# Kernel optimization log

Measured on AMD Instinct MI355X. Metric: run time of the kernel, lower is better.

Reference implementation:

```python
import jax, jax.numpy as jnp
import numpy as np

B, N, C, IC = 8, 4096, 1024, 256
EPS = 1e-5


def setup_inputs() -> dict:
    key = jax.random.key(0)
    ks = jax.random.split(key, 10)
    s = 0.02  # keep activations well-scaled
    return {
        "v": jax.random.normal(ks[0], (B, N, C), jnp.float32),
        "g_w": jax.random.normal(ks[1], (IC, C), jnp.float32) * s,
        "g_b": jax.random.normal(ks[2], (IC,), jnp.float32) * s,
        "theta_w": jax.random.normal(ks[3], (IC, C), jnp.float32) * s,
        "theta_b": jax.random.normal(ks[4], (IC,), jnp.float32) * s,
        "phi_w": jax.random.normal(ks[5], (IC, C), jnp.float32) * s,
        "phi_b": jax.random.normal(ks[6], (IC,), jnp.float32) * s,
        "W_w": jax.random.normal(ks[7], (C, IC), jnp.float32) * s,
        "W_b": jax.random.normal(ks[8], (C,), jnp.float32) * s,
        "bn_gamma": jnp.ones((C,), jnp.float32),
        "bn_beta": jnp.zeros((C,), jnp.float32),
    }


def reference(v, g_w, g_b, theta_w, theta_b, phi_w, phi_b, W_w, W_b, bn_gamma, bn_beta):
    # v: (B, N, C). All Conv1d(k=1) == per-token matmul.
    g_v = jnp.einsum("bnc,ic->bni", v, g_w) + g_b          # (B, N, IC)
    theta_v = jnp.einsum("bnc,ic->bni", v, theta_w) + theta_b
    phi_v = jnp.einsum("bnc,ic->bni", v, phi_w) + phi_b
    n = v.shape[1]
    # Affinity: R = theta @ phi^T, normalized by N (no softmax)
    R = jnp.einsum("bni,bmi->bnm", theta_v, phi_v) / n      # (B, N, N)
    y = jnp.einsum("bnm,bmi->bni", R, g_v)                  # (B, N, IC)
    W_y = jnp.einsum("bni,ci->bnc", y, W_w) + W_b           # (B, N, C)
    # BatchNorm1d training mode: per-channel stats over (B, N), biased var
    mean = jnp.mean(W_y, axis=(0, 1))
    var = jnp.var(W_y, axis=(0, 1))
    W_y = (W_y - mean) * jax.lax.rsqrt(var + EPS) * bn_gamma + bn_beta
    return W_y + v                                          # residual, (B, N, C)
```

## Files before the change

### kernel.cpp

```cpp
#include <hip/hip_runtime.h>
#include <hip/hip_bf16.h>
#include <stdint.h>


using bf16 = __hip_bfloat16;
typedef __attribute__((ext_vector_type(8))) short short8;
typedef __attribute__((ext_vector_type(4))) float f32x4;
typedef __attribute__((ext_vector_type(4))) short short4v;

#define DEVI static __device__ __forceinline__

DEVI float bf2f(unsigned short u) {
  union { unsigned int i; float f; } x; x.i = ((unsigned int)u) << 16; return x.f;
}
DEVI unsigned short f2bf(float f) {
  __hip_bfloat16 h = __float2bfloat16(f);
  return *reinterpret_cast<unsigned short*>(&h);
}

DEVI void gld16(const void* g, void* l) {
  __builtin_amdgcn_global_load_lds((__attribute__((address_space(1))) void*)g,
                                   (__attribute__((address_space(3))) void*)l,
                                   16, 0, 0);
}

DEVI short8 cvt8(float4 a, float4 b) {
  short8 o;
  o[0] = (short)f2bf(a.x); o[1] = (short)f2bf(a.y);
  o[2] = (short)f2bf(a.z); o[3] = (short)f2bf(a.w);
  o[4] = (short)f2bf(b.x); o[5] = (short)f2bf(b.y);
  o[6] = (short)f2bf(b.z); o[7] = (short)f2bf(b.w);
  return o;
}

DEVI void mfma_loop(const bf16* A, int ldA, const bf16* B, int ldB,
                    int kiters, bf16* lds_a, bf16* lds_b, f32x4 acc[4][4])
{
  const int tid = threadIdx.x;
  const int lane = tid & 63;
  const int w = tid >> 6;
  const int wr = w >> 1, wc = w & 1;
  const int srow = w * 32 + (lane >> 2);
  const int scol = (lane & 3) * 8;
  const bf16* ga0 = A + (size_t)srow * ldA + scol;
  const bf16* ga1 = A + (size_t)(srow + 16) * ldA + scol;
  const bf16* gb0 = B + (size_t)srow * ldB + scol;
  const bf16* gb1 = B + (size_t)(srow + 16) * ldB + scol;
  bf16* la0 = lds_a + w * 1024 + lane * 8;
  bf16* la1 = la0 + 512;
  bf16* lb0 = lds_b + w * 1024 + lane * 8;
  bf16* lb1 = lb0 + 512;
  const int frow = lane & 15;
  const int fk = (lane >> 4) * 8;
  const bf16* ra = lds_a + (wr * 64 + frow) * 32 + fk;
  const bf16* rb = lds_b + (wc * 64 + frow) * 32 + fk;
  for (int it = 0; it < kiters; ++it) {
    gld16(ga0, la0); gld16(ga1, la1);
    gld16(gb0, lb0); gld16(gb1, lb1);
    ga0 += 32; ga1 += 32; gb0 += 32; gb1 += 32;
    __syncthreads();
    short8 af[4], bfr[4];
#pragma unroll
    for (int i = 0; i < 4; ++i) af[i] = *(const short8*)(ra + i * 512);
#pragma unroll
    for (int j = 0; j < 4; ++j) bfr[j] = *(const short8*)(rb + j * 512);
#pragma unroll
    for (int i = 0; i < 4; ++i)
#pragma unroll
      for (int j = 0; j < 4; ++j)
        acc[i][j] = __builtin_amdgcn_mfma_f32_16x16x32_bf16(af[i], bfr[j], acc[i][j], 0, 0, 0);
    __syncthreads();
  }
}

#define ACC_INIT(acc)                                   \
  _Pragma("unroll") for (int i = 0; i < 4; ++i)         \
  _Pragma("unroll") for (int j = 0; j < 4; ++j)         \
      acc[i][j] = (f32x4){0.f, 0.f, 0.f, 0.f};

__global__ __launch_bounds__(256) void k_cast_all(
    const float* __restrict__ v, bf16* __restrict__ vbf,
    const float* __restrict__ s0, const float* __restrict__ s1,
    const float* __restrict__ s2, const float* __restrict__ s3,
    bf16* __restrict__ d0, bf16* __restrict__ d1,
    bf16* __restrict__ d2, bf16* __restrict__ d3)
{
  const float* in; bf16* out; size_t base;
  const int bx = blockIdx.x;
  if (bx < 16384) {
    in = v; out = vbf; base = (size_t)bx * 2048;
  } else {
    const int wq = bx - 16384;
    switch (wq >> 7) {
      case 0:  in = s0; out = d0; break;
      case 1:  in = s1; out = d1; break;
      case 2:  in = s2; out = d2; break;
      default: in = s3; out = d3; break;
    }
    base = (size_t)(wq & 127) * 2048;
  }
  const size_t idx = base + (size_t)threadIdx.x * 8;
  float4 a = *(const float4*)(in + idx);
  float4 b = *(const float4*)(in + idx + 4);
  *(short8*)(out + idx) = cvt8(a, b);
}

__global__ __launch_bounds__(256) void k_proj(
    const bf16* __restrict__ vbf,
    const bf16* __restrict__ w_th, const float* __restrict__ b_th,
    const bf16* __restrict__ w_ph, const float* __restrict__ b_ph,
    const bf16* __restrict__ w_g,  const float* __restrict__ b_g,
    bf16* __restrict__ theta, bf16* __restrict__ phiT, bf16* __restrict__ gT)
{
  __shared__ __align__(16) char smem[34048];
  bf16* lds_a = (bf16*)smem;
  bf16* lds_b = (bf16*)(smem + 8192);
  unsigned short* lds_t = (unsigned short*)smem;

  const int tt = blockIdx.x;
  const int yy = blockIdx.y;
  const int proj = yy >> 1;
  const int icb = (yy & 1) * 128;
  const bf16* wsel = (proj == 0) ? w_th : ((proj == 1) ? w_ph : w_g);
  const float* bsel = (proj == 0) ? b_th : ((proj == 1) ? b_ph : b_g);

  const size_t t0 = (size_t)tt * 128;
  f32x4 acc[4][4];
  ACC_INIT(acc);
  mfma_loop(vbf + t0 * 1024, 1024, wsel + (size_t)icb * 1024, 1024, 32, lds_a, lds_b, acc);

  const int tid = threadIdx.x, lane = tid & 63, w = tid >> 6;
  const int wr = w >> 1, wc = w & 1, quad = lane >> 4, l15 = lane & 15;
  float biasv[4];
#pragma unroll
  for (int j = 0; j < 4; ++j) biasv[j] = bsel[icb + wc * 64 + j * 16 + l15];

  if (proj == 0) {
#pragma unroll
    for (int i = 0; i < 4; ++i)
#pragma unroll
      for (int j = 0; j < 4; ++j)
#pragma unroll
        for (int r = 0; r < 4; ++r) {
          int m = wr * 64 + i * 16 + quad * 4 + r;
          int n = wc * 64 + j * 16 + l15;
          theta[(t0 + m) * 256 + icb + n] = __float2bfloat16(acc[i][j][r] + biasv[j]);
        }
  } else {
#pragma unroll
    for (int i = 0; i < 4; ++i)
#pragma unroll
      for (int j = 0; j < 4; ++j)
#pragma unroll
        for (int r = 0; r < 4; ++r) {
          int m = wr * 64 + i * 16 + quad * 4 + r;
          int n = wc * 64 + j * 16 + l15;
          lds_t[m * 133 + n] = f2bf(acc[i][j][r] + biasv[j]);
        }
    __syncthreads();
    bf16* outT = (proj == 1) ? phiT : gT;
    const int bb = (int)(t0 >> 12);
    const int n0 = (int)(t0 & 4095);
    const int tg = tid & 7;
    const int ch0 = tid >> 3;
#pragma unroll
    for (int half = 0; half < 2; ++half)
#pragma unroll
      for (int cc = 0; cc < 4; ++cc) {
        int ch = ch0 + cc * 32;
        int tok0 = half * 64 + tg * 8;
        short8 pk;
#pragma unroll
        for (int r = 0; r < 8; ++r) pk[r] = (short)lds_t[(tok0 + r) * 133 + ch];
        *(short8*)(outT + ((size_t)(bb * 256 + icb + ch)) * 4096 + n0 + tok0) = pk;
      }
  }
}

__global__ __launch_bounds__(256) void k_affin(
    const bf16* __restrict__ phiT, const bf16* __restrict__ gT, float* __restrict__ M)
{
  __shared__ __align__(16) char smem[16384];
  bf16* lds_a = (bf16*)smem;
  bf16* lds_b = (bf16*)(smem + 8192);
  const int kc = blockIdx.x;
  const int jt = blockIdx.y >> 1;
  const int it2 = blockIdx.y & 1;
  const int bb = blockIdx.z;
  f32x4 acc[4][4];
  ACC_INIT(acc);
  const bf16* A = phiT + ((size_t)bb * 256 + jt * 128) * 4096 + kc * 512;
  const bf16* B = gT   + ((size_t)bb * 256 + it2 * 128) * 4096 + kc * 512;
  mfma_loop(A, 4096, B, 4096, 16, lds_a, lds_b, acc);
  const int tid = threadIdx.x, lane = tid & 63, w = tid >> 6;
  const int wr = w >> 1, wc = w & 1, quad = lane >> 4, l15 = lane & 15;
  float* Mb = M + (size_t)bb * 65536;
#pragma unroll
  for (int i = 0; i < 4; ++i)
#pragma unroll
    for (int j = 0; j < 4; ++j)
#pragma unroll
      for (int r = 0; r < 4; ++r) {
        int m = wr * 64 + i * 16 + quad * 4 + r;
        int n = wc * 64 + j * 16 + l15;
        atomicAdd(&Mb[(size_t)(jt * 128 + m) * 256 + it2 * 128 + n], acc[i][j][r]);
      }
}

__global__ __launch_bounds__(256) void k_mconv(const float* __restrict__ M, bf16* __restrict__ Mbf)
{
  int i = blockIdx.x * 256 + threadIdx.x;
  Mbf[i] = __float2bfloat16(M[i] * (1.0f / 4096.0f));
}

__global__ __launch_bounds__(256) void k_pt(
    const bf16* __restrict__ Ww, const bf16* __restrict__ Mbf, bf16* __restrict__ PT)
{
  __shared__ __align__(16) char smem[16384];
  bf16* lds_a = (bf16*)smem;
  bf16* lds_b = (bf16*)(smem + 8192);
  const int ct = blockIdx.x;
  const int jt = blockIdx.y;
  const int bb = blockIdx.z;
  f32x4 acc[4][4];
  ACC_INIT(acc);
  mfma_loop(Ww + (size_t)ct * 128 * 256, 256,
            Mbf + ((size_t)bb * 256 + jt * 128) * 256, 256, 8, lds_a, lds_b, acc);
  const int tid = threadIdx.x, lane = tid & 63, w = tid >> 6;
  const int wr = w >> 1, wc = w & 1, quad = lane >> 4, l15 = lane & 15;
#pragma unroll
  for (int i = 0; i < 4; ++i)
#pragma unroll
    for (int j = 0; j < 4; ++j)
#pragma unroll
      for (int r = 0; r < 4; ++r) {
        int m = wr * 64 + i * 16 + quad * 4 + r;
        int n = wc * 64 + j * 16 + l15;
        PT[((size_t)bb * 1024 + ct * 128 + m) * 256 + jt * 128 + n] = __float2bfloat16(acc[i][j][r]);
      }
}

__global__ __launch_bounds__(256) void k_wy(
    const bf16* __restrict__ theta, const bf16* __restrict__ PT, bf16* __restrict__ Wy,
    float* __restrict__ sums, float* __restrict__ sumsq)
{
  __shared__ __align__(16) char smem[16384];
  bf16* lds_a = (bf16*)smem;
  bf16* lds_b = (bf16*)(smem + 8192);
  const size_t t0 = (size_t)blockIdx.x * 128;
  const int ct = blockIdx.y;
  const int bb = (int)(t0 >> 12);
  f32x4 acc[4][4];
  ACC_INIT(acc);
  mfma_loop(theta + t0 * 256, 256,
            PT + ((size_t)bb * 1024 + ct * 128) * 256, 256, 8, lds_a, lds_b, acc);
  const int tid = threadIdx.x, lane = tid & 63, w = tid >> 6;
  const int wr = w >> 1, wc = w & 1, quad = lane >> 4, l15 = lane & 15;
  float ps[4] = {0.f, 0.f, 0.f, 0.f}, pq[4] = {0.f, 0.f, 0.f, 0.f};
#pragma unroll
  for (int i = 0; i < 4; ++i)
#pragma unroll
    for (int j = 0; j < 4; ++j)
#pragma unroll
      for (int r = 0; r < 4; ++r) {
        int m = wr * 64 + i * 16 + quad * 4 + r;
        int n = wc * 64 + j * 16 + l15;
        float f = acc[i][j][r];
        Wy[(t0 + m) * 1024 + ct * 128 + n] = __float2bfloat16(f);
        ps[j] += f; pq[j] += f * f;
      }
#pragma unroll
  for (int j = 0; j < 4; ++j) {
    ps[j] += __shfl_xor(ps[j], 16); ps[j] += __shfl_xor(ps[j], 32);
    pq[j] += __shfl_xor(pq[j], 16); pq[j] += __shfl_xor(pq[j], 32);
  }
  if (quad == 0) {
#pragma unroll
    for (int j = 0; j < 4; ++j) {
      int c = ct * 128 + wc * 64 + j * 16 + l15;
      atomicAdd(&sums[c], ps[j]);
      atomicAdd(&sumsq[c], pq[j]);
    }
  }
}

__global__ __launch_bounds__(256) void k_out(const bf16* __restrict__ Wy, const float* __restrict__ v,
                                             const float* __restrict__ sums, const float* __restrict__ sumsq,
                                             const float* __restrict__ gamma, const float* __restrict__ beta,
                                             float* __restrict__ out)
{
  const size_t idx = ((size_t)blockIdx.x * 256 + threadIdx.x) * 4;
  const int c = (int)(idx & 1023);
  float4 sm = *(const float4*)(sums + c);
  float4 sq = *(const float4*)(sumsq + c);
  float4 gm = *(const float4*)(gamma + c);
  float4 bt = *(const float4*)(beta + c);
  short4v wv = *(const short4v*)(Wy + idx);
  float4 vv = *(const float4*)(v + idx);
  float4 o;
#pragma unroll
  for (int k = 0; k < 4; ++k) {
    float smk = (&sm.x)[k], sqk = (&sq.x)[k], gmk = (&gm.x)[k], btk = (&bt.x)[k];
    float mean = smk * (1.0f / 32768.0f);
    float var = sqk * (1.0f / 32768.0f) - mean * mean;
    float sc = gmk * rsqrtf(var + 1e-5f);
    float sh = btk - mean * sc;
    (&o.x)[k] = bf2f((unsigned short)wv[k]) * sc + sh + (&vv.x)[k];
  }
  *(float4*)(out + idx) = o;
}

extern "C" void kernel_launch(void* const* d_in, const int* in_sizes, int n_in,
                              void* d_out, int out_size, void* d_ws, size_t ws_size,
                              hipStream_t stream)
{
  (void)in_sizes; (void)n_in; (void)out_size; (void)ws_size;
  const float* v    = (const float*)d_in[0];
  const float* g_w  = (const float*)d_in[1];
  const float* g_b  = (const float*)d_in[2];
  const float* th_w = (const float*)d_in[3];
  const float* th_b = (const float*)d_in[4];
  const float* ph_w = (const float*)d_in[5];
  const float* ph_b = (const float*)d_in[6];
  const float* W_w  = (const float*)d_in[7];
  const float* gamma = (const float*)d_in[9];
  const float* beta  = (const float*)d_in[10];
  float* out = (float*)d_out;

  char* ws = (char*)d_ws;
  bf16* vbf  = (bf16*)ws;
  bf16* Wy   = (bf16*)ws;
  ws += (size_t)32768 * 1024 * 2;
  bf16* theta = (bf16*)ws;  ws += (size_t)32768 * 256 * 2;
  bf16* phiT  = (bf16*)ws;  ws += (size_t)32768 * 256 * 2;
  bf16* gT    = (bf16*)ws;  ws += (size_t)32768 * 256 * 2;
  float* M    = (float*)ws; ws += (size_t)8 * 65536 * 4;
  bf16* Mbf   = (bf16*)ws;  ws += (size_t)8 * 65536 * 2;
  bf16* PT    = (bf16*)ws;  ws += (size_t)8 * 1024 * 256 * 2;
  bf16* thwb  = (bf16*)ws;  ws += (size_t)256 * 1024 * 2;
  bf16* phwb  = (bf16*)ws;  ws += (size_t)256 * 1024 * 2;
  bf16* gwb   = (bf16*)ws;  ws += (size_t)256 * 1024 * 2;
  bf16* Wwb   = (bf16*)ws;  ws += (size_t)1024 * 256 * 2;
  float* sums = (float*)ws; ws += 4096;
  float* sumsq= (float*)ws; ws += 4096;

  hipMemsetAsync(M, 0, (size_t)8 * 65536 * 4, stream);
  hipMemsetAsync(sums, 0, 8192, stream);

  k_cast_all<<<16384 + 512, 256, 0, stream>>>(v, vbf, th_w, ph_w, g_w, W_w,
                                              thwb, phwb, gwb, Wwb);

  k_proj <<<dim3(256, 6), 256, 0, stream>>>(vbf, thwb, th_b, phwb, ph_b, gwb, g_b, theta, phiT, gT);
  k_affin<<<dim3(8, 4, 8), 256, 0, stream>>>(phiT, gT, M);
  k_mconv<<<2048, 256, 0, stream>>>(M, Mbf);
  k_pt   <<<dim3(8, 2, 8), 256, 0, stream>>>(Wwb, Mbf, PT);
  k_wy   <<<dim3(256, 8), 256, 0, stream>>>(theta, PT, Wy, sums, sumsq);
  k_out  <<<32768, 256, 0, stream>>>(Wy, v, sums, sumsq, gamma, beta, out);
}
```

Measured before the change: 471.2 us.

## Swizzle LDS tile columns and replace split-K atomics with partial-sum reduction

The shared GEMM loop now XOR-swizzles the 16-byte column chunk by row on both the global-to-LDS store side and the fragment-read side, to cut LDS bank conflicts. The affinity kernel writes each K-chunk's partial tile to its own buffer instead of issuing float atomicAdds, and the conversion kernel sums the eight partials with vector loads before scaling and casting to bf16. This drops the memset and the atomic contention. In exchange it adds extra partial-buffer traffic, and that buffer reuses the vbf/Wy workspace region, which relies on vbf being dead by then.

```diff
diff --git a/kernel.cpp b/kernel.cpp
--- a/kernel.cpp
+++ b/kernel.cpp
@@ -41,7 +41,7 @@
   const int w = tid >> 6;
   const int wr = w >> 1, wc = w & 1;
   const int srow = w * 32 + (lane >> 2);
-  const int scol = (lane & 3) * 8;
+  const int scol = (((lane & 3) ^ ((srow >> 1) & 3))) * 8;
   const bf16* ga0 = A + (size_t)srow * ldA + scol;
   const bf16* ga1 = A + (size_t)(srow + 16) * ldA + scol;
   const bf16* gb0 = B + (size_t)srow * ldB + scol;
@@ -51,7 +51,7 @@
   bf16* lb0 = lds_b + w * 1024 + lane * 8;
   bf16* lb1 = lb0 + 512;
   const int frow = lane & 15;
-  const int fk = (lane >> 4) * 8;
+  const int fk = (((lane >> 4) ^ ((frow >> 1) & 3))) * 8;
   const bf16* ra = lds_a + (wr * 64 + frow) * 32 + fk;
   const bf16* rb = lds_b + (wc * 64 + frow) * 32 + fk;
   for (int it = 0; it < kiters; ++it) {
@@ -178,7 +178,7 @@
 }
 
 __global__ __launch_bounds__(256) void k_affin(
-    const bf16* __restrict__ phiT, const bf16* __restrict__ gT, float* __restrict__ M)
+    const bf16* __restrict__ phiT, const bf16* __restrict__ gT, float* __restrict__ Mp)
 {
   __shared__ __align__(16) char smem[16384];
   bf16* lds_a = (bf16*)smem;
@@ -194,7 +194,7 @@
   mfma_loop(A, 4096, B, 4096, 16, lds_a, lds_b, acc);
   const int tid = threadIdx.x, lane = tid & 63, w = tid >> 6;
   const int wr = w >> 1, wc = w & 1, quad = lane >> 4, l15 = lane & 15;
-  float* Mb = M + (size_t)bb * 65536;
+  float* Mb = Mp + ((size_t)kc * 8 + bb) * 65536;
 #pragma unroll
   for (int i = 0; i < 4; ++i)
 #pragma unroll
@@ -203,14 +203,25 @@
       for (int r = 0; r < 4; ++r) {
         int m = wr * 64 + i * 16 + quad * 4 + r;
         int n = wc * 64 + j * 16 + l15;
-        atomicAdd(&Mb[(size_t)(jt * 128 + m) * 256 + it2 * 128 + n], acc[i][j][r]);
+        Mb[(size_t)(jt * 128 + m) * 256 + it2 * 128 + n] = acc[i][j][r];
       }
 }
 
-__global__ __launch_bounds__(256) void k_mconv(const float* __restrict__ M, bf16* __restrict__ Mbf)
-{
-  int i = blockIdx.x * 256 + threadIdx.x;
-  Mbf[i] = __float2bfloat16(M[i] * (1.0f / 4096.0f));
+__global__ __launch_bounds__(256) void k_mconv(const float* __restrict__ Mp, bf16* __restrict__ Mbf)
+{
+  const size_t i = ((size_t)blockIdx.x * 256 + threadIdx.x) * 4;
+  float4 s = *(const float4*)(Mp + i);
+#pragma unroll
+  for (int kc = 1; kc < 8; ++kc) {
+    float4 p = *(const float4*)(Mp + (size_t)kc * 524288 + i);
+    s.x += p.x; s.y += p.y; s.z += p.z; s.w += p.w;
+  }
+  short4v o;
+  o[0] = (short)f2bf(s.x * (1.0f / 4096.0f));
+  o[1] = (short)f2bf(s.y * (1.0f / 4096.0f));
+  o[2] = (short)f2bf(s.z * (1.0f / 4096.0f));
+  o[3] = (short)f2bf(s.w * (1.0f / 4096.0f));
+  *(short4v*)(Mbf + i) = o;
 }
 
 __global__ __launch_bounds__(256) void k_pt(
@@ -330,11 +341,11 @@
   char* ws = (char*)d_ws;
   bf16* vbf  = (bf16*)ws;
   bf16* Wy   = (bf16*)ws;
+  float* Mp  = (float*)ws;
   ws += (size_t)32768 * 1024 * 2;
   bf16* theta = (bf16*)ws;  ws += (size_t)32768 * 256 * 2;
   bf16* phiT  = (bf16*)ws;  ws += (size_t)32768 * 256 * 2;
   bf16* gT    = (bf16*)ws;  ws += (size_t)32768 * 256 * 2;
-  float* M    = (float*)ws; ws += (size_t)8 * 65536 * 4;
   bf16* Mbf   = (bf16*)ws;  ws += (size_t)8 * 65536 * 2;
   bf16* PT    = (bf16*)ws;  ws += (size_t)8 * 1024 * 256 * 2;
   bf16* thwb  = (bf16*)ws;  ws += (size_t)256 * 1024 * 2;
@@ -344,15 +355,14 @@
   float* sums = (float*)ws; ws += 4096;
   float* sumsq= (float*)ws; ws += 4096;
 
-  hipMemsetAsync(M, 0, (size_t)8 * 65536 * 4, stream);
   hipMemsetAsync(sums, 0, 8192, stream);
 
   k_cast_all<<<16384 + 512, 256, 0, stream>>>(v, vbf, th_w, ph_w, g_w, W_w,
                                               thwb, phwb, gwb, Wwb);
 
   k_proj <<<dim3(256, 6), 256, 0, stream>>>(vbf, thwb, th_b, phwb, ph_b, gwb, g_b, theta, phiT, gT);
-  k_affin<<<dim3(8, 4, 8), 256, 0, stream>>>(phiT, gT, M);
-  k_mconv<<<2048, 256, 0, stream>>>(M, Mbf);
+  k_affin<<<dim3(8, 4, 8), 256, 0, stream>>>(phiT, gT, Mp);
+  k_mconv<<<512, 256, 0, stream>>>(Mp, Mbf);
   k_pt   <<<dim3(8, 2, 8), 256, 0, stream>>>(Wwb, Mbf, PT);
   k_wy   <<<dim3(256, 8), 256, 0, stream>>>(theta, PT, Wy, sums, sumsq);
   k_out  <<<32768, 256, 0, stream>>>(Wy, v, sums, sumsq, gamma, beta, out);
```

After: 451.6 us. -4.2%, faster.
